# Kernel tuning notes

Hardware: AMD Instinct MI355X
Metric: run time of the kernel (lower is better)

Reference implementation:

```python
import jax, jax.numpy as jnp
import numpy as np

HORIZON_K = 20
EPS = 1e-8


def _unfold_gather(x, time_idx, k):
    # Emulates zero-pad + tensor.unfold(1, k, 1).permute(3,0,1,2) + index_select(2, time_idx)
    # x: [N, T-1, C] -> [k, N, S, C] where out[ki, n, s] = x_padded[n, time_idx[s] + ki]
    N, Tm1, C = x.shape
    xp = jnp.concatenate([x, jnp.zeros((N, k, C), x.dtype)], axis=1)
    gidx = time_idx[None, :] + jnp.arange(k)[:, None]  # [k, S]
    return jnp.transpose(xp[:, gidx, :], (1, 0, 2, 3))  # [k, N, S, C]


def _gru_rollout(x_seq, h0, W_ih, W_hh, b_ih, b_hh):
    # x_seq: [k, B, A]; h0: [B, H]; torch GRU gate order: r, z, n
    H = h0.shape[-1]
    def step(h, x):
        gi = x @ W_ih.T + b_ih          # [B, 3H]
        gh = h @ W_hh.T + b_hh          # [B, 3H]
        r = jax.nn.sigmoid(gi[:, :H] + gh[:, :H])
        z = jax.nn.sigmoid(gi[:, H:2 * H] + gh[:, H:2 * H])
        n = jnp.tanh(gi[:, 2 * H:] + r * gh[:, 2 * H:])
        hn = (1.0 - z) * n + z * h
        return hn, hn
    _, hs = jax.lax.scan(step, h0, x_seq)
    return hs  # [k, B, H]


def _mlp(x, W1, b1, W2, b2, W3, b3):
    x = jax.nn.relu(x @ W1 + b1)
    x = jax.nn.relu(x @ W2 + b2)
    return x @ W3 + b3


def _l2norm(x):
    n = jnp.linalg.norm(x, axis=-1, keepdims=True)
    return x / jnp.maximum(n, EPS)


def setup_inputs() -> dict:
    key = jax.random.key(0)
    ks = jax.random.split(key, 16)
    N, T, H, A, M = 1024, 128, 256, 18, 512
    g = lambda k, sh, s: jax.random.normal(k, sh, jnp.float32) * s
    return {
        "actions": jax.random.randint(ks[0], (N, T), 0, A),
        "dones": jnp.zeros((N, T), jnp.float32),
        "b_t": g(ks[1], (N * T, H), 1.0),
        "z_t": g(ks[2], (N * T, H), 1.0),
        "time_subsample": jax.random.randint(ks[3], (6,), 0, T - 1),
        "unroll_subsample": jax.random.randint(ks[4], (2,), 0, HORIZON_K),
        "W_ih": g(ks[5], (3 * H, A), 0.05), "W_hh": g(ks[6], (3 * H, H), 0.05),
        "b_ih": g(ks[7], (3 * H,), 0.05), "b_hh": g(ks[8], (3 * H,), 0.05),
        "W1": g(ks[9], (H, M), 0.05), "b1": g(ks[10], (M,), 0.05),
        "W2": g(ks[11], (M, M), 0.05), "b2": g(ks[12], (M,), 0.05),
        "W3": g(ks[13], (M, H), 0.05), "b3": g(ks[14], (H,), 0.05),
    }


def reference(actions, dones, b_t, z_t, time_subsample, unroll_subsample,
              W_ih, W_hh, b_ih, b_hh, W1, b1, W2, b2, W3, b3):
    N, T = actions.shape
    H = b_t.shape[-1]
    A = W_ih.shape[1]
    k = HORIZON_K

    # mask (dones fixed to all-zero -> max_k == horizon_k)
    not_dones = (1.0 - dones).reshape(N, T, 1)
    nd_unf = _unfold_gather(not_dones[:, :-1], time_subsample, k)        # [k,N,S,1]
    fmask = jnp.cumprod(nd_unf, axis=0).reshape(k, -1, 1)                # [k,N*S,1]
    fmask = (fmask[unroll_subsample] > 0).astype(jnp.float32)            # [F,B,1]

    # unfolded one-hot actions
    onehot = jax.nn.one_hot(actions, A, dtype=jnp.float32)               # [N,T,A]
    act_unf = _unfold_gather(onehot[:, :-1], time_subsample, k)          # [k,N,S,A]
    act_unf = act_unf.reshape(k, -1, A)                                  # [k,B,A]

    # GRU initial states from core outputs at subsampled times
    c = b_t.reshape(N, T, H)[:, :-1][:, time_subsample]                  # [N,S,H]
    h0 = c.reshape(-1, H)                                                # [B,H]

    # 20-step open-loop GRU rollout
    h_pred = _gru_rollout(act_unf, h0, W_ih, W_hh, b_ih, b_hh)           # [k,B,H]
    h_pred = h_pred[unroll_subsample]                                    # [F,B,H]

    final_pred = _mlp(h_pred, W1, b1, W2, b2, W3, b3)                    # [F,B,H]
    norm = jnp.linalg.norm(final_pred, axis=2)
    reg = 0.02 * jnp.square(norm - 1.0)                                  # [F,B]
    final_pred = _l2norm(final_pred)

    # targets (no grad): unfolded future encodings, normalized
    z = jax.lax.stop_gradient(z_t).reshape(N, T, -1)
    tgt = _unfold_gather(z[:, 1:], time_subsample, k)                    # [k,N,S,C]
    tgt = tgt[unroll_subsample].reshape(len(unroll_subsample), -1, z.shape[-1])
    tgt = _l2norm(tgt)                                                   # [F,B,C]

    loss = jnp.square(final_pred - tgt)                                  # [F,B,C]
    loss = loss.mean(-1, keepdims=True)                                  # [F,B,1]
    loss = jnp.sum(loss * fmask) / jnp.maximum(jnp.sum(fmask), 1.0)
    return loss + reg.mean()
```

## Files before the change

### kernel.cpp

```cpp
#include <hip/hip_runtime.h>
#include <hip/hip_bf16.h>
#include <math.h>

#define NN 1024
#define TT 128
#define SS 6
#define FF 2
#define HH 256
#define AA 18
#define MM 512
#define KH 20
#define BB (NN*SS)
#define RR (FF*BB)

#define SCL_RZ (-1.44269504089f)
#define SCL_N  (-2.88539008178f)
#define TBL_STRIDE 784

typedef __bf16 bf16x8 __attribute__((ext_vector_type(8)));
typedef float f32x4 __attribute__((ext_vector_type(4)));

__device__ __forceinline__ f32x4 mfma16(bf16x8 a, bf16x8 b, f32x4 c) {
    return __builtin_amdgcn_mfma_f32_16x16x32_bf16(a, b, c, 0, 0, 0);
}
__device__ __forceinline__ unsigned short f2b(float f) {
    return __builtin_bit_cast(unsigned short, __float2bfloat16(f));
}
__device__ __forceinline__ float b2f(unsigned short u) {
    return __builtin_bit_cast(float, (unsigned)u << 16);
}
__device__ __forceinline__ float rcp_f(float x)  { return __builtin_amdgcn_rcpf(x); }
__device__ __forceinline__ float exp2_f(float x) { return __builtin_amdgcn_exp2f(x); }

#define OFF_ACT   0UL
#define OFF_HPRED 491520UL
#define OFF_WHH   6782976UL
#define OFF_W1T   7176192UL
#define OFF_W2T   7438336UL
#define OFF_W3T   7962624UL
#define OFF_TBL   8224768UL
#define OFF_PART  8284352UL

__global__ void k_prep(const float* __restrict__ Whh, const float* __restrict__ W1,
                       const float* __restrict__ W2, const float* __restrict__ W3,
                       const float* __restrict__ Wih, const float* __restrict__ bih,
                       const float* __restrict__ bhh,
                       const int* __restrict__ actions, const int* __restrict__ ts,
                       unsigned short* whh_s, unsigned short* w1t, unsigned short* w2t,
                       unsigned short* w3t, float* tbl, int* act) {
    int idx = blockIdx.x * 256 + threadIdx.x;
    if (idx < 196608) {
        int wrow = idx >> 8;
        float scl = (wrow < 512) ? SCL_RZ : SCL_N;
        whh_s[idx] = f2b(Whh[idx] * scl);
        return;
    }
    idx -= 196608;
    if (idx < 131072) { int m = idx >> 8, k = idx & 255; w1t[idx] = f2b(W1[k * MM + m]); return; }
    idx -= 131072;
    if (idx < 262144) { int m = idx >> 9, k = idx & 511; w2t[idx] = f2b(W2[k * MM + m]); return; }
    idx -= 262144;
    if (idx < 131072) { int c = idx >> 9, k = idx & 511; w3t[idx] = f2b(W3[k * HH + c]); return; }
    idx -= 131072;
    if (idx < 19 * TBL_STRIDE) {
        int a = idx / TBL_STRIDE, rem = idx - a * TBL_STRIDE;
        float v = 0.f;
        if (rem < 768) {
            int g = rem >> 8;
            float scl = (g < 2) ? SCL_RZ : SCL_N;
            float w = (a < AA) ? Wih[rem * AA + a] : 0.f;
            v = scl * (w + bih[rem] + ((g < 2) ? bhh[rem] : 0.f));
        }
        tbl[idx] = v;
        return;
    }
    idx -= 19 * TBL_STRIDE;
    if (idx < BB * KH) {
        int b = idx / KH, k = idx - b * KH;
        int n = b / SS, s = b - n * SS;
        int tt = ts[s] + k;
        act[idx] = (tt < TT - 1) ? actions[n * TT + tt] : AA;
    }
}

__global__ void __launch_bounds__(512, 2)
k_gru_all(const unsigned short* __restrict__ whh_s, const float* __restrict__ tblg,
          const float* __restrict__ bhh, const int* __restrict__ actg,
          const int* __restrict__ us, const int* __restrict__ ts,
          const float* __restrict__ b_t, unsigned short* __restrict__ hpred) {
    __shared__ float tbl[19 * TBL_STRIDE];
    __shared__ unsigned short htile[2][32][264];
    __shared__ int act_l[24][KH];

    int tid = threadIdx.x, wave = tid >> 6, lane = tid & 63;
    int l15 = lane & 15, grp = lane >> 4, lk8 = grp << 3, r4 = grp << 2;
    int rb = blockIdx.x * 24;
    int u0 = us[0], u1 = us[1];
    int kmax = u0 > u1 ? u0 : u1;

    for (int i = tid; i < 19 * TBL_STRIDE / 4; i += 512)
        reinterpret_cast<float4*>(tbl)[i] = reinterpret_cast<const float4*>(tblg)[i];
    if (tid < 24 * KH) {
        int r = tid / KH, k2 = tid - r * KH;
        act_l[r][k2] = actg[(rb + r) * KH + k2];
    }

    for (int i = tid; i < 2 * 32 * 32; i += 512) {
        int buf = i >> 10, rem = i & 1023, row = rem >> 5, c8 = (rem & 31) << 3;
        uint4 pk = {0u, 0u, 0u, 0u};
        if (buf == 0 && row < 24) {
            int b = rb + row;
            int n = b / SS, s = b - n * SS;
            const float* src = &b_t[(size_t)(n * TT + ts[s]) * HH + c8];
            pk.x = f2b(src[0]) | ((unsigned)f2b(src[1]) << 16);
            pk.y = f2b(src[2]) | ((unsigned)f2b(src[3]) << 16);
            pk.z = f2b(src[4]) | ((unsigned)f2b(src[5]) << 16);
            pk.w = f2b(src[6]) | ((unsigned)f2b(src[7]) << 16);
        }
        *reinterpret_cast<uint4*>(&htile[buf][row][c8]) = pk;
    }

    bf16x8 wr[6][8];
#pragma unroll
    for (int ct = 0; ct < 6; ++ct) {
        int wrow = (ct >> 1) * 256 + wave * 32 + (ct & 1) * 16 + l15;
        const unsigned short* base = &whh_s[(size_t)wrow * HH];
#pragma unroll
        for (int kk = 0; kk < 8; ++kk)
            wr[ct][kk] = *reinterpret_cast<const bf16x8*>(&base[kk * 32 + lk8]);
    }
    float bhn[2];
#pragma unroll
    for (int cj = 0; cj < 2; ++cj) bhn[cj] = SCL_N * bhh[512 + wave * 32 + cj * 16 + l15];
    __syncthreads();

    int cur = 0;
    for (int ki = 0; ki <= kmax; ++ki) {
        int nxt = cur ^ 1;
#pragma unroll
        for (int rt = 0; rt < 2; ++rt) {
            f32x4 aR[2] = {}, aZ[2] = {}, aN[2] = {};
#pragma unroll
            for (int kk = 0; kk < 8; ++kk) {
                bf16x8 ah = *reinterpret_cast<const bf16x8*>(&htile[cur][rt * 16 + l15][kk * 32 + lk8]);
                aR[0] = mfma16(ah, wr[0][kk], aR[0]);
                aR[1] = mfma16(ah, wr[1][kk], aR[1]);
                aZ[0] = mfma16(ah, wr[2][kk], aZ[0]);
                aZ[1] = mfma16(ah, wr[3][kk], aZ[1]);
                aN[0] = mfma16(ah, wr[4][kk], aN[0]);
                aN[1] = mfma16(ah, wr[5][kk], aN[1]);
            }
#pragma unroll
            for (int cj = 0; cj < 2; ++cj) {
                int j2 = wave * 32 + cj * 16 + l15;
                float bhnv = bhn[cj];
#pragma unroll
                for (int reg = 0; reg < 4; ++reg) {
                    int rowl = rt * 16 + r4 + reg;
                    if (rt == 0 || rowl < 24) {
                        const float* tb = &tbl[act_l[rowl][ki] * TBL_STRIDE];
                        float r = rcp_f(1.f + exp2_f(aR[cj][reg] + tb[j2]));
                        float z = rcp_f(1.f + exp2_f(aZ[cj][reg] + tb[256 + j2]));
                        float ghn = aN[cj][reg] + bhnv;
                        float nv = 2.f * rcp_f(1.f + exp2_f(tb[512 + j2] + r * ghn)) - 1.f;
                        float h = b2f(htile[cur][rowl][j2]);
                        float hn2 = nv + z * (h - nv);
                        unsigned short hbv = f2b(hn2);
                        htile[nxt][rowl][j2] = hbv;
                        if (ki == u0) hpred[(size_t)(rb + rowl) * HH + j2] = hbv;
                        if (ki == u1) hpred[(size_t)(BB + rb + rowl) * HH + j2] = hbv;
                    }
                }
            }
        }
        __syncthreads();
        cur = nxt;
    }
}

__device__ __forceinline__ int xsw(int row, int chunk) {
    return (row << 9) + ((chunk ^ (row & 7)) << 3);
}

__global__ void __launch_bounds__(512, 4)
k_mlp_loss(const unsigned short* __restrict__ hpred, const unsigned short* __restrict__ w1t,
           const unsigned short* __restrict__ w2t, const unsigned short* __restrict__ w3t,
           const float* __restrict__ b1, const float* __restrict__ b2,
           const float* __restrict__ b3, const float* __restrict__ z_t,
           const float* __restrict__ dones, const int* __restrict__ ts,
           const int* __restrict__ us, float* __restrict__ part) {
    __shared__ unsigned short xs[48 * 512];
    __shared__ unsigned short zs[48 * 256];
    __shared__ float rstat[48][8][3];
    __shared__ float vmask[48];

    int tid = threadIdx.x, wave = tid >> 6, lane = tid & 63;
    int l15 = lane & 15, grp = lane >> 4, lk8 = grp << 3, r4 = grp << 2;
    int rb = blockIdx.x * 48;

    if (tid < 48) {
        int rg = rb + tid;
        int f = rg >= BB ? 1 : 0;
        int b = rg - f * BB;
        int n = b / SS, s = b - n * SS;
        int t = ts[s], u = us[f];
        float m = (t + u < TT - 1) ? 1.f : 0.f;
        if (m > 0.f) for (int j = 0; j <= u; ++j) m *= (1.f - dones[n * TT + t + j]);
        vmask[tid] = (m > 0.f) ? 1.f : 0.f;
    }
    for (int i = tid; i < 48 * 64; i += 512) {
        int row = i >> 6, c4 = (i & 63) << 2;
        int rg = rb + row;
        int f = rg >= BB ? 1 : 0;
        int b = rg - f * BB;
        int n = b / SS, s = b - n * SS;
        int t = ts[s], u = us[f];
        uint2 pk = {0u, 0u};
        if (t + u < TT - 1) {
            float4 v = *reinterpret_cast<const float4*>(&z_t[(size_t)(n * TT + 1 + t + u) * HH + c4]);
            pk.x = f2b(v.x) | ((unsigned)f2b(v.y) << 16);
            pk.y = f2b(v.z) | ((unsigned)f2b(v.w) << 16);
        }
        *reinterpret_cast<uint2*>(&zs[row * 256 + c4]) = pk;
    }

    {
        f32x4 acc[3][4] = {};
        for (int kk = 0; kk < 8; ++kk) {
            int k0 = kk * 32 + lk8;
            bf16x8 av[3];
#pragma unroll
            for (int rt = 0; rt < 3; ++rt)
                av[rt] = *reinterpret_cast<const bf16x8*>(&hpred[(size_t)(rb + rt * 16 + l15) * HH + k0]);
#pragma unroll
            for (int ct = 0; ct < 4; ++ct) {
                int col = wave * 64 + ct * 16 + l15;
                bf16x8 bv = *reinterpret_cast<const bf16x8*>(&w1t[(size_t)col * HH + k0]);
#pragma unroll
                for (int rt = 0; rt < 3; ++rt) acc[rt][ct] = mfma16(av[rt], bv, acc[rt][ct]);
            }
        }
#pragma unroll
        for (int ct = 0; ct < 4; ++ct) {
            int col = wave * 64 + ct * 16 + l15;
            float bb = b1[col];
#pragma unroll
            for (int rt = 0; rt < 3; ++rt)
#pragma unroll
                for (int reg = 0; reg < 4; ++reg)
                    xs[xsw(rt * 16 + r4 + reg, col >> 3) + (col & 7)] =
                        f2b(fmaxf(acc[rt][ct][reg] + bb, 0.f));
        }
    }
    __syncthreads();

    {
        f32x4 acc[3][4] = {};
        for (int kk = 0; kk < 16; ++kk) {
            bf16x8 av[3];
#pragma unroll
            for (int rt = 0; rt < 3; ++rt)
                av[rt] = *reinterpret_cast<const bf16x8*>(&xs[xsw(rt * 16 + l15, kk * 4 + grp)]);
#pragma unroll
            for (int ct = 0; ct < 4; ++ct) {
                int col = wave * 64 + ct * 16 + l15;
                bf16x8 bv = *reinterpret_cast<const bf16x8*>(&w2t[(size_t)col * MM + kk * 32 + lk8]);
#pragma unroll
                for (int rt = 0; rt < 3; ++rt) acc[rt][ct] = mfma16(av[rt], bv, acc[rt][ct]);
            }
        }
        __syncthreads();
#pragma unroll
        for (int ct = 0; ct < 4; ++ct) {
            int col = wave * 64 + ct * 16 + l15;
            float bb = b2[col];
#pragma unroll
            for (int rt = 0; rt < 3; ++rt)
#pragma unroll
                for (int reg = 0; reg < 4; ++reg)
                    xs[xsw(rt * 16 + r4 + reg, col >> 3) + (col & 7)] =
                        f2b(fmaxf(acc[rt][ct][reg] + bb, 0.f));
        }
    }
    __syncthreads();

    {
        f32x4 acc[3][2] = {};
        for (int kk = 0; kk < 16; ++kk) {
            bf16x8 av[3];
#pragma unroll
            for (int rt = 0; rt < 3; ++rt)
                av[rt] = *reinterpret_cast<const bf16x8*>(&xs[xsw(rt * 16 + l15, kk * 4 + grp)]);
#pragma unroll
            for (int ct = 0; ct < 2; ++ct) {
                int col = wave * 32 + ct * 16 + l15;
                bf16x8 bv = *reinterpret_cast<const bf16x8*>(&w3t[(size_t)col * MM + kk * 32 + lk8]);
#pragma unroll
                for (int rt = 0; rt < 3; ++rt) acc[rt][ct] = mfma16(av[rt], bv, acc[rt][ct]);
            }
        }
        float b3c0 = b3[wave * 32 + l15];
        float b3c1 = b3[wave * 32 + 16 + l15];
#pragma unroll
        for (int rt = 0; rt < 3; ++rt)
#pragma unroll
            for (int reg = 0; reg < 4; ++reg) {
                int row = rt * 16 + r4 + reg;
                float p0 = acc[rt][0][reg] + b3c0;
                float p1 = acc[rt][1][reg] + b3c1;
                float z0 = b2f(zs[row * 256 + wave * 32 + l15]);
                float z1 = b2f(zs[row * 256 + wave * 32 + 16 + l15]);
                float psq = p0 * p0 + p1 * p1;
                float zsq = z0 * z0 + z1 * z1;
                float pz  = p0 * z0 + p1 * z1;
#pragma unroll
                for (int o = 1; o < 16; o <<= 1) {
                    psq += __shfl_xor(psq, o);
                    zsq += __shfl_xor(zsq, o);
                    pz  += __shfl_xor(pz, o);
                }
                if (l15 == 0) {
                    rstat[row][wave][0] = psq;
                    rstat[row][wave][1] = zsq;
                    rstat[row][wave][2] = pz;
                }
            }
    }
    __syncthreads();

    if (tid < 64) {
        float a0 = 0.f, a1 = 0.f, a2 = 0.f;
        if (tid < 48) {
            float sp = 0.f, sz = 0.f, spz = 0.f;
#pragma unroll
            for (int w = 0; w < 8; ++w) {
                sp  += rstat[tid][w][0];
                sz  += rstat[tid][w][1];
                spz += rstat[tid][w][2];
            }
            float npn = sqrtf(sp), nzn = sqrtf(sz);
            float d = npn - 1.f;
            a2 = 0.02f * d * d;
            float mp = fmaxf(npn, 1e-8f), mz = fmaxf(nzn, 1e-8f);
            float lossr = (sp / (mp * mp) + sz / (mz * mz) - 2.f * spz / (mp * mz)) * (1.f / HH);
            float vm = vmask[tid];
            a0 = vm * lossr;
            a1 = vm;
        }
#pragma unroll
        for (int o = 1; o < 64; o <<= 1) {
            a0 += __shfl_xor(a0, o);
            a1 += __shfl_xor(a1, o);
            a2 += __shfl_xor(a2, o);
        }
        if (tid == 0) {
            part[blockIdx.x * 3 + 0] = a0;
            part[blockIdx.x * 3 + 1] = a1;
            part[blockIdx.x * 3 + 2] = a2;
        }
    }
}

__global__ void k_final(const float* __restrict__ part, float* out) {
    int tid = threadIdx.x, wave = tid >> 6, lane = tid & 63;
    float s0 = 0.f, s1 = 0.f, s2 = 0.f;
    for (int i = tid; i < 256; i += 256) {
        s0 += part[i * 3 + 0];
        s1 += part[i * 3 + 1];
        s2 += part[i * 3 + 2];
    }
    for (int o = 32; o; o >>= 1) {
        s0 += __shfl_xor(s0, o);
        s1 += __shfl_xor(s1, o);
        s2 += __shfl_xor(s2, o);
    }
    __shared__ float sm[4][3];
    if (lane == 0) { sm[wave][0] = s0; sm[wave][1] = s1; sm[wave][2] = s2; }
    __syncthreads();
    if (tid == 0) {
        float a = 0.f, b = 0.f, c = 0.f;
        for (int w = 0; w < 4; ++w) { a += sm[w][0]; b += sm[w][1]; c += sm[w][2]; }
        out[0] = a / fmaxf(b, 1.f) + c * (1.f / RR);
    }
}

extern "C" void kernel_launch(void* const* d_in, const int* in_sizes, int n_in,
                              void* d_out, int out_size, void* d_ws, size_t ws_size,
                              hipStream_t stream) {
    const int*   actions = (const int*)d_in[0];
    const float* dones   = (const float*)d_in[1];
    const float* b_t     = (const float*)d_in[2];
    const float* z_t     = (const float*)d_in[3];
    const int*   ts      = (const int*)d_in[4];
    const int*   us      = (const int*)d_in[5];
    const float* W_ih    = (const float*)d_in[6];
    const float* W_hh    = (const float*)d_in[7];
    const float* b_ih    = (const float*)d_in[8];
    const float* b_hh    = (const float*)d_in[9];
    const float* W1      = (const float*)d_in[10];
    const float* b1      = (const float*)d_in[11];
    const float* W2      = (const float*)d_in[12];
    const float* b2      = (const float*)d_in[13];
    const float* W3      = (const float*)d_in[14];
    const float* b3      = (const float*)d_in[15];

    char* ws = (char*)d_ws;
    int*            act   = (int*)(ws + OFF_ACT);
    unsigned short* hpred = (unsigned short*)(ws + OFF_HPRED);
    unsigned short* whh_s = (unsigned short*)(ws + OFF_WHH);
    unsigned short* w1t   = (unsigned short*)(ws + OFF_W1T);
    unsigned short* w2t   = (unsigned short*)(ws + OFF_W2T);
    unsigned short* w3t   = (unsigned short*)(ws + OFF_W3T);
    float*          tbl   = (float*)(ws + OFF_TBL);
    float*          part  = (float*)(ws + OFF_PART);

    k_prep<<<3355, 256, 0, stream>>>(W_hh, W1, W2, W3, W_ih, b_ih, b_hh, actions, ts,
                                     whh_s, w1t, w2t, w3t, tbl, act);
    k_gru_all<<<256, 512, 0, stream>>>(whh_s, tbl, b_hh, act, us, ts, b_t, hpred);
    k_mlp_loss<<<256, 512, 0, stream>>>(hpred, w1t, w2t, w3t, b1, b2, b3,
                                        z_t, dones, ts, us, part);
    k_final<<<1, 256, 0, stream>>>(part, (float*)d_out);
}
```

Before: 115.1 us.

## Compute GRU input gates via one-hot MFMA instead of LDS lookup table

Replaces the ~60KB shared-memory W_ih/bias lookup table with a bf16 packed W_ih (bias folded in as an extra column). The input-gate contributions are now produced by MFMA against a one-hot action vector built in registers. It also reassigns output columns so each lane owns two adjacent hidden units, keeps the fp32 hidden state in registers instead of re-reading bf16 from LDS, and writes packed 32-bit stores. The goal is to free LDS for occupancy and remove gather loads from the recurrence, at the cost of extra MFMAs per step and bf16 rounding of the input weights.

```diff
diff --git a/kernel.cpp b/kernel.cpp
--- a/kernel.cpp
+++ b/kernel.cpp
@@ -15,10 +15,10 @@
 
 #define SCL_RZ (-1.44269504089f)
 #define SCL_N  (-2.88539008178f)
-#define TBL_STRIDE 784
 
 typedef __bf16 bf16x8 __attribute__((ext_vector_type(8)));
 typedef float f32x4 __attribute__((ext_vector_type(4)));
+typedef unsigned ux4 __attribute__((ext_vector_type(4)));
 
 __device__ __forceinline__ f32x4 mfma16(bf16x8 a, bf16x8 b, f32x4 c) {
     return __builtin_amdgcn_mfma_f32_16x16x32_bf16(a, b, c, 0, 0, 0);
@@ -38,8 +38,8 @@
 #define OFF_W1T   7176192UL
 #define OFF_W2T   7438336UL
 #define OFF_W3T   7962624UL
-#define OFF_TBL   8224768UL
-#define OFF_PART  8284352UL
+#define OFF_WIHP  8224768UL
+#define OFF_PART  8273920UL
 
 __global__ void k_prep(const float* __restrict__ Whh, const float* __restrict__ W1,
                        const float* __restrict__ W2, const float* __restrict__ W3,
@@ -47,7 +47,7 @@
                        const float* __restrict__ bhh,
                        const int* __restrict__ actions, const int* __restrict__ ts,
                        unsigned short* whh_s, unsigned short* w1t, unsigned short* w2t,
-                       unsigned short* w3t, float* tbl, int* act) {
+                       unsigned short* w3t, unsigned short* wihp, int* act_t) {
     int idx = blockIdx.x * 256 + threadIdx.x;
     if (idx < 196608) {
         int wrow = idx >> 8;
@@ -62,48 +62,68 @@
     idx -= 262144;
     if (idx < 131072) { int c = idx >> 9, k = idx & 511; w3t[idx] = f2b(W3[k * HH + c]); return; }
     idx -= 131072;
-    if (idx < 19 * TBL_STRIDE) {
-        int a = idx / TBL_STRIDE, rem = idx - a * TBL_STRIDE;
+    if (idx < 24576) {
+        int c = idx >> 5, k = idx & 31;
+        int g = c >> 8;
+        float scl = (g < 2) ? SCL_RZ : SCL_N;
         float v = 0.f;
-        if (rem < 768) {
-            int g = rem >> 8;
-            float scl = (g < 2) ? SCL_RZ : SCL_N;
-            float w = (a < AA) ? Wih[rem * AA + a] : 0.f;
-            v = scl * (w + bih[rem] + ((g < 2) ? bhh[rem] : 0.f));
-        }
-        tbl[idx] = v;
+        if (k < AA) v = scl * Wih[c * AA + k];
+        else if (k == AA) v = scl * (bih[c] + ((g < 2) ? bhh[c] : 0.f));
+        wihp[idx] = f2b(v);
         return;
     }
-    idx -= 19 * TBL_STRIDE;
-    if (idx < BB * KH) {
-        int b = idx / KH, k = idx - b * KH;
+    idx -= 24576;
+    if (idx < KH * BB) {
+        int ki = idx / BB, b = idx - ki * BB;
         int n = b / SS, s = b - n * SS;
-        int tt = ts[s] + k;
-        act[idx] = (tt < TT - 1) ? actions[n * TT + tt] : AA;
+        int tt = ts[s] + ki;
+        act_t[idx] = (tt < TT - 1) ? actions[n * TT + tt] : AA;
     }
 }
 
 __global__ void __launch_bounds__(512, 2)
-k_gru_all(const unsigned short* __restrict__ whh_s, const float* __restrict__ tblg,
-          const float* __restrict__ bhh, const int* __restrict__ actg,
+k_gru_all(const unsigned short* __restrict__ whh_s, const unsigned short* __restrict__ wihp,
+          const float* __restrict__ bhh, const int* __restrict__ act_t,
           const int* __restrict__ us, const int* __restrict__ ts,
           const float* __restrict__ b_t, unsigned short* __restrict__ hpred) {
-    __shared__ float tbl[19 * TBL_STRIDE];
-    __shared__ unsigned short htile[2][32][264];
-    __shared__ int act_l[24][KH];
+    __shared__ alignas(16) unsigned short htile[2][32][264];
 
     int tid = threadIdx.x, wave = tid >> 6, lane = tid & 63;
     int l15 = lane & 15, grp = lane >> 4, lk8 = grp << 3, r4 = grp << 2;
     int rb = blockIdx.x * 24;
     int u0 = us[0], u1 = us[1];
     int kmax = u0 > u1 ? u0 : u1;
-
-    for (int i = tid; i < 19 * TBL_STRIDE / 4; i += 512)
-        reinterpret_cast<float4*>(tbl)[i] = reinterpret_cast<const float4*>(tblg)[i];
-    if (tid < 24 * KH) {
-        int r = tid / KH, k2 = tid - r * KH;
-        act_l[r][k2] = actg[(rb + r) * KH + k2];
-    }
+    int j0 = wave * 32 + 2 * l15;
+
+    bf16x8 wr[6][8];
+    bf16x8 wih[6];
+#pragma unroll
+    for (int ct = 0; ct < 6; ++ct) {
+        int wrow = (ct >> 1) * 256 + j0 + (ct & 1);
+        const unsigned short* base = &whh_s[(size_t)wrow * HH];
+#pragma unroll
+        for (int kk = 0; kk < 8; ++kk)
+            wr[ct][kk] = *reinterpret_cast<const bf16x8*>(&base[kk * 32 + lk8]);
+        wih[ct] = *reinterpret_cast<const bf16x8*>(&wihp[wrow * 32 + lk8]);
+    }
+    float bhn0 = SCL_N * bhh[512 + j0];
+    float bhn1 = SCL_N * bhh[512 + j0 + 1];
+
+    float hm[2][2][4];
+#pragma unroll
+    for (int rt = 0; rt < 2; ++rt)
+#pragma unroll
+        for (int reg = 0; reg < 4; ++reg) {
+            int rowl = rt * 16 + r4 + reg;
+            float v0 = 0.f, v1 = 0.f;
+            if (rowl < 24) {
+                int b = rb + rowl;
+                int n = b / SS, s = b - n * SS;
+                const float* src = &b_t[(size_t)(n * TT + ts[s]) * HH + j0];
+                v0 = src[0]; v1 = src[1];
+            }
+            hm[rt][0][reg] = v0; hm[rt][1][reg] = v1;
+        }
 
     for (int i = tid; i < 2 * 32 * 32; i += 512) {
         int buf = i >> 10, rem = i & 1023, row = rem >> 5, c8 = (rem & 31) << 3;
@@ -119,57 +139,60 @@
         }
         *reinterpret_cast<uint4*>(&htile[buf][row][c8]) = pk;
     }
-
-    bf16x8 wr[6][8];
-#pragma unroll
-    for (int ct = 0; ct < 6; ++ct) {
-        int wrow = (ct >> 1) * 256 + wave * 32 + (ct & 1) * 16 + l15;
-        const unsigned short* base = &whh_s[(size_t)wrow * HH];
-#pragma unroll
-        for (int kk = 0; kk < 8; ++kk)
-            wr[ct][kk] = *reinterpret_cast<const bf16x8*>(&base[kk * 32 + lk8]);
-    }
-    float bhn[2];
-#pragma unroll
-    for (int cj = 0; cj < 2; ++cj) bhn[cj] = SCL_N * bhh[512 + wave * 32 + cj * 16 + l15];
     __syncthreads();
 
     int cur = 0;
     for (int ki = 0; ki <= kmax; ++ki) {
         int nxt = cur ^ 1;
+        int a0 = act_t[ki * BB + rb + l15];
+        int i1 = rb + 16 + l15;
+        int a1 = act_t[ki * BB + (i1 < BB ? i1 : BB - 1)];
+
 #pragma unroll
         for (int rt = 0; rt < 2; ++rt) {
-            f32x4 aR[2] = {}, aZ[2] = {}, aN[2] = {};
+            int a = rt ? a1 : a0;
+            ux4 ohu;
+#pragma unroll
+            for (int i = 0; i < 4; ++i) {
+                int k0 = lk8 + 2 * i, k1 = k0 + 1;
+                unsigned v0 = (a == k0 || k0 == AA) ? 0x3F80u : 0u;
+                unsigned v1 = (a == k1 || k1 == AA) ? 0x3F80u : 0u;
+                ohu[i] = v0 | (v1 << 16);
+            }
+            bf16x8 ohf = __builtin_bit_cast(bf16x8, ohu);
+
+            f32x4 aR0 = {}, aR1 = {}, aZ0 = {}, aZ1 = {}, aN0 = {}, aN1 = {}, aNI0 = {}, aNI1 = {};
+            aR0  = mfma16(ohf, wih[0], aR0);  aR1  = mfma16(ohf, wih[1], aR1);
+            aZ0  = mfma16(ohf, wih[2], aZ0);  aZ1  = mfma16(ohf, wih[3], aZ1);
+            aNI0 = mfma16(ohf, wih[4], aNI0); aNI1 = mfma16(ohf, wih[5], aNI1);
 #pragma unroll
             for (int kk = 0; kk < 8; ++kk) {
                 bf16x8 ah = *reinterpret_cast<const bf16x8*>(&htile[cur][rt * 16 + l15][kk * 32 + lk8]);
-                aR[0] = mfma16(ah, wr[0][kk], aR[0]);
-                aR[1] = mfma16(ah, wr[1][kk], aR[1]);
-                aZ[0] = mfma16(ah, wr[2][kk], aZ[0]);
-                aZ[1] = mfma16(ah, wr[3][kk], aZ[1]);
-                aN[0] = mfma16(ah, wr[4][kk], aN[0]);
-                aN[1] = mfma16(ah, wr[5][kk], aN[1]);
-            }
-#pragma unroll
-            for (int cj = 0; cj < 2; ++cj) {
-                int j2 = wave * 32 + cj * 16 + l15;
-                float bhnv = bhn[cj];
-#pragma unroll
-                for (int reg = 0; reg < 4; ++reg) {
-                    int rowl = rt * 16 + r4 + reg;
-                    if (rt == 0 || rowl < 24) {
-                        const float* tb = &tbl[act_l[rowl][ki] * TBL_STRIDE];
-                        float r = rcp_f(1.f + exp2_f(aR[cj][reg] + tb[j2]));
-                        float z = rcp_f(1.f + exp2_f(aZ[cj][reg] + tb[256 + j2]));
-                        float ghn = aN[cj][reg] + bhnv;
-                        float nv = 2.f * rcp_f(1.f + exp2_f(tb[512 + j2] + r * ghn)) - 1.f;
-                        float h = b2f(htile[cur][rowl][j2]);
-                        float hn2 = nv + z * (h - nv);
-                        unsigned short hbv = f2b(hn2);
-                        htile[nxt][rowl][j2] = hbv;
-                        if (ki == u0) hpred[(size_t)(rb + rowl) * HH + j2] = hbv;
-                        if (ki == u1) hpred[(size_t)(BB + rb + rowl) * HH + j2] = hbv;
-                    }
+                aR0 = mfma16(ah, wr[0][kk], aR0); aR1 = mfma16(ah, wr[1][kk], aR1);
+                aZ0 = mfma16(ah, wr[2][kk], aZ0); aZ1 = mfma16(ah, wr[3][kk], aZ1);
+                aN0 = mfma16(ah, wr[4][kk], aN0); aN1 = mfma16(ah, wr[5][kk], aN1);
+            }
+#pragma unroll
+            for (int reg = 0; reg < 4; ++reg) {
+                int rowl = rt * 16 + r4 + reg;
+                float r0 = rcp_f(1.f + exp2_f(aR0[reg]));
+                float r1 = rcp_f(1.f + exp2_f(aR1[reg]));
+                float z0 = rcp_f(1.f + exp2_f(aZ0[reg]));
+                float z1 = rcp_f(1.f + exp2_f(aZ1[reg]));
+                float tv0 = aNI0[reg] + r0 * (aN0[reg] + bhn0);
+                float tv1 = aNI1[reg] + r1 * (aN1[reg] + bhn1);
+                float nv0 = 2.f * rcp_f(1.f + exp2_f(tv0)) - 1.f;
+                float nv1 = 2.f * rcp_f(1.f + exp2_f(tv1)) - 1.f;
+                float h0n = nv0 + z0 * (hm[rt][0][reg] - nv0);
+                float h1n = nv1 + z1 * (hm[rt][1][reg] - nv1);
+                hm[rt][0][reg] = h0n; hm[rt][1][reg] = h1n;
+                if (rowl < 24) {
+                    unsigned hv = (unsigned)f2b(h0n) | ((unsigned)f2b(h1n) << 16);
+                    *reinterpret_cast<unsigned*>(&htile[nxt][rowl][j0]) = hv;
+                    if (ki == u0)
+                        *reinterpret_cast<unsigned*>(&hpred[(size_t)(rb + rowl) * HH + j0]) = hv;
+                    if (ki == u1)
+                        *reinterpret_cast<unsigned*>(&hpred[(size_t)(BB + rb + rowl) * HH + j0]) = hv;
                 }
             }
         }
@@ -364,10 +387,10 @@
 __global__ void k_final(const float* __restrict__ part, float* out) {
     int tid = threadIdx.x, wave = tid >> 6, lane = tid & 63;
     float s0 = 0.f, s1 = 0.f, s2 = 0.f;
-    for (int i = tid; i < 256; i += 256) {
-        s0 += part[i * 3 + 0];
-        s1 += part[i * 3 + 1];
-        s2 += part[i * 3 + 2];
+    if (tid < 256) {
+        s0 = part[tid * 3 + 0];
+        s1 = part[tid * 3 + 1];
+        s2 = part[tid * 3 + 2];
     }
     for (int o = 32; o; o >>= 1) {
         s0 += __shfl_xor(s0, o);
@@ -405,18 +428,18 @@
     const float* b3      = (const float*)d_in[15];
 
     char* ws = (char*)d_ws;
-    int*            act   = (int*)(ws + OFF_ACT);
+    int*            act_t = (int*)(ws + OFF_ACT);
     unsigned short* hpred = (unsigned short*)(ws + OFF_HPRED);
     unsigned short* whh_s = (unsigned short*)(ws + OFF_WHH);
     unsigned short* w1t   = (unsigned short*)(ws + OFF_W1T);
     unsigned short* w2t   = (unsigned short*)(ws + OFF_W2T);
     unsigned short* w3t   = (unsigned short*)(ws + OFF_W3T);
-    float*          tbl   = (float*)(ws + OFF_TBL);
+    unsigned short* wihp  = (unsigned short*)(ws + OFF_WIHP);
     float*          part  = (float*)(ws + OFF_PART);
 
-    k_prep<<<3355, 256, 0, stream>>>(W_hh, W1, W2, W3, W_ih, b_ih, b_hh, actions, ts,
-                                     whh_s, w1t, w2t, w3t, tbl, act);
-    k_gru_all<<<256, 512, 0, stream>>>(whh_s, tbl, b_hh, act, us, ts, b_t, hpred);
+    k_prep<<<3392, 256, 0, stream>>>(W_hh, W1, W2, W3, W_ih, b_ih, b_hh, actions, ts,
+                                     whh_s, w1t, w2t, w3t, wihp, act_t);
+    k_gru_all<<<256, 512, 0, stream>>>(whh_s, wihp, b_hh, act_t, us, ts, b_t, hpred);
     k_mlp_loss<<<256, 512, 0, stream>>>(hpred, w1t, w2t, w3t, b1, b2, b3,
                                         z_t, dones, ts, us, part);
     k_final<<<1, 256, 0, stream>>>(part, (float*)d_out);
```

After: 133.9 us. 1.16x slower.

## Shrink GRU blocks to 16 rows, keep hidden state in fp32 registers

Applied to the files above, without the earlier changes.

The GRU rollout kernel now handles 16 batch rows per block instead of 24, which removes the wasted half-filled second MFMA row tile and raises the grid from 256 to 384 blocks to spread work across more CUs. The hidden state is carried in fp32 registers rather than reread from a bf16 LDS tile, and the double-buffered tile is replaced by one buffer with an extra barrier between the MFMA reads and the writes. This trades an added sync per step and a repeated per-block table load for better CU utilisation, and may slightly change numerics because h no longer round-trips through bf16. k_final is also simplified to a direct load per thread.

```diff
diff --git a/kernel.cpp b/kernel.cpp
--- a/kernel.cpp
+++ b/kernel.cpp
@@ -89,35 +89,20 @@
           const int* __restrict__ us, const int* __restrict__ ts,
           const float* __restrict__ b_t, unsigned short* __restrict__ hpred) {
     __shared__ float tbl[19 * TBL_STRIDE];
-    __shared__ unsigned short htile[2][32][264];
-    __shared__ int act_l[24][KH];
+    __shared__ int act_l[16][KH];
+    __shared__ unsigned short htile[16][264];
 
     int tid = threadIdx.x, wave = tid >> 6, lane = tid & 63;
     int l15 = lane & 15, grp = lane >> 4, lk8 = grp << 3, r4 = grp << 2;
-    int rb = blockIdx.x * 24;
+    int rb = blockIdx.x * 16;
     int u0 = us[0], u1 = us[1];
     int kmax = u0 > u1 ? u0 : u1;
 
     for (int i = tid; i < 19 * TBL_STRIDE / 4; i += 512)
         reinterpret_cast<float4*>(tbl)[i] = reinterpret_cast<const float4*>(tblg)[i];
-    if (tid < 24 * KH) {
-        int r = tid / KH, k2 = tid - r * KH;
-        act_l[r][k2] = actg[(rb + r) * KH + k2];
-    }
-
-    for (int i = tid; i < 2 * 32 * 32; i += 512) {
-        int buf = i >> 10, rem = i & 1023, row = rem >> 5, c8 = (rem & 31) << 3;
-        uint4 pk = {0u, 0u, 0u, 0u};
-        if (buf == 0 && row < 24) {
-            int b = rb + row;
-            int n = b / SS, s = b - n * SS;
-            const float* src = &b_t[(size_t)(n * TT + ts[s]) * HH + c8];
-            pk.x = f2b(src[0]) | ((unsigned)f2b(src[1]) << 16);
-            pk.y = f2b(src[2]) | ((unsigned)f2b(src[3]) << 16);
-            pk.z = f2b(src[4]) | ((unsigned)f2b(src[5]) << 16);
-            pk.w = f2b(src[6]) | ((unsigned)f2b(src[7]) << 16);
-        }
-        *reinterpret_cast<uint4*>(&htile[buf][row][c8]) = pk;
+    if (tid < 16 * KH) {
+        int r = tid / KH, k = tid - r * KH;
+        act_l[r][k] = actg[(rb + r) * KH + k];
     }
 
     bf16x8 wr[6][8];
@@ -129,52 +114,70 @@
         for (int kk = 0; kk < 8; ++kk)
             wr[ct][kk] = *reinterpret_cast<const bf16x8*>(&base[kk * 32 + lk8]);
     }
+
+    float hm[2][4];
+#pragma unroll
+    for (int cj = 0; cj < 2; ++cj)
+#pragma unroll
+        for (int reg = 0; reg < 4; ++reg) {
+            int b = rb + r4 + reg;
+            int n = b / SS, s = b - n * SS;
+            hm[cj][reg] = b_t[(size_t)(n * TT + ts[s]) * HH + wave * 32 + cj * 16 + l15];
+        }
     float bhn[2];
 #pragma unroll
     for (int cj = 0; cj < 2; ++cj) bhn[cj] = SCL_N * bhh[512 + wave * 32 + cj * 16 + l15];
+
+    {
+        int row = tid >> 5, c8 = (tid & 31) << 3;
+        int b = rb + row;
+        int n = b / SS, s = b - n * SS;
+        const float* src = &b_t[(size_t)(n * TT + ts[s]) * HH + c8];
+        uint4 pk;
+        pk.x = f2b(src[0]) | ((unsigned)f2b(src[1]) << 16);
+        pk.y = f2b(src[2]) | ((unsigned)f2b(src[3]) << 16);
+        pk.z = f2b(src[4]) | ((unsigned)f2b(src[5]) << 16);
+        pk.w = f2b(src[6]) | ((unsigned)f2b(src[7]) << 16);
+        *reinterpret_cast<uint4*>(&htile[row][c8]) = pk;
+    }
     __syncthreads();
 
-    int cur = 0;
     for (int ki = 0; ki <= kmax; ++ki) {
-        int nxt = cur ^ 1;
-#pragma unroll
-        for (int rt = 0; rt < 2; ++rt) {
-            f32x4 aR[2] = {}, aZ[2] = {}, aN[2] = {};
-#pragma unroll
-            for (int kk = 0; kk < 8; ++kk) {
-                bf16x8 ah = *reinterpret_cast<const bf16x8*>(&htile[cur][rt * 16 + l15][kk * 32 + lk8]);
-                aR[0] = mfma16(ah, wr[0][kk], aR[0]);
-                aR[1] = mfma16(ah, wr[1][kk], aR[1]);
-                aZ[0] = mfma16(ah, wr[2][kk], aZ[0]);
-                aZ[1] = mfma16(ah, wr[3][kk], aZ[1]);
-                aN[0] = mfma16(ah, wr[4][kk], aN[0]);
-                aN[1] = mfma16(ah, wr[5][kk], aN[1]);
-            }
-#pragma unroll
-            for (int cj = 0; cj < 2; ++cj) {
-                int j2 = wave * 32 + cj * 16 + l15;
-                float bhnv = bhn[cj];
-#pragma unroll
-                for (int reg = 0; reg < 4; ++reg) {
-                    int rowl = rt * 16 + r4 + reg;
-                    if (rt == 0 || rowl < 24) {
-                        const float* tb = &tbl[act_l[rowl][ki] * TBL_STRIDE];
-                        float r = rcp_f(1.f + exp2_f(aR[cj][reg] + tb[j2]));
-                        float z = rcp_f(1.f + exp2_f(aZ[cj][reg] + tb[256 + j2]));
-                        float ghn = aN[cj][reg] + bhnv;
-                        float nv = 2.f * rcp_f(1.f + exp2_f(tb[512 + j2] + r * ghn)) - 1.f;
-                        float h = b2f(htile[cur][rowl][j2]);
-                        float hn2 = nv + z * (h - nv);
-                        unsigned short hbv = f2b(hn2);
-                        htile[nxt][rowl][j2] = hbv;
-                        if (ki == u0) hpred[(size_t)(rb + rowl) * HH + j2] = hbv;
-                        if (ki == u1) hpred[(size_t)(BB + rb + rowl) * HH + j2] = hbv;
-                    }
-                }
-            }
+        f32x4 aR[2] = {}, aZ[2] = {}, aN[2] = {};
+#pragma unroll
+        for (int kk = 0; kk < 8; ++kk) {
+            bf16x8 ah = *reinterpret_cast<const bf16x8*>(&htile[l15][kk * 32 + lk8]);
+            aR[0] = mfma16(ah, wr[0][kk], aR[0]);
+            aR[1] = mfma16(ah, wr[1][kk], aR[1]);
+            aZ[0] = mfma16(ah, wr[2][kk], aZ[0]);
+            aZ[1] = mfma16(ah, wr[3][kk], aZ[1]);
+            aN[0] = mfma16(ah, wr[4][kk], aN[0]);
+            aN[1] = mfma16(ah, wr[5][kk], aN[1]);
         }
         __syncthreads();
-        cur = nxt;
+
+#pragma unroll
+        for (int cj = 0; cj < 2; ++cj) {
+            int j2 = wave * 32 + cj * 16 + l15;
+            float bhnv = bhn[cj];
+#pragma unroll
+            for (int reg = 0; reg < 4; ++reg) {
+                int row = r4 + reg;
+                const float* tb = &tbl[act_l[row][ki] * TBL_STRIDE];
+                float r = rcp_f(1.f + exp2_f(aR[cj][reg] + tb[j2]));
+                float z = rcp_f(1.f + exp2_f(aZ[cj][reg] + tb[256 + j2]));
+                float ghn = aN[cj][reg] + bhnv;
+                float nv = 2.f * rcp_f(1.f + exp2_f(tb[512 + j2] + r * ghn)) - 1.f;
+                float h = hm[cj][reg];
+                float hn2 = nv + z * (h - nv);
+                hm[cj][reg] = hn2;
+                unsigned short hbv = f2b(hn2);
+                htile[row][j2] = hbv;
+                if (ki == u0) hpred[(size_t)(rb + row) * HH + j2] = hbv;
+                if (ki == u1) hpred[(size_t)(BB + rb + row) * HH + j2] = hbv;
+            }
+        }
+        __syncthreads();
     }
 }
 
@@ -205,7 +208,7 @@
         int n = b / SS, s = b - n * SS;
         int t = ts[s], u = us[f];
         float m = (t + u < TT - 1) ? 1.f : 0.f;
-        if (m > 0.f) for (int j = 0; j <= u; ++j) m *= (1.f - dones[n * TT + t + j]);
+        if (m > 0.f) for (int jj = 0; jj <= u; ++jj) m *= (1.f - dones[n * TT + t + jj]);
         vmask[tid] = (m > 0.f) ? 1.f : 0.f;
     }
     for (int i = tid; i < 48 * 64; i += 512) {
@@ -363,12 +366,9 @@
 
 __global__ void k_final(const float* __restrict__ part, float* out) {
     int tid = threadIdx.x, wave = tid >> 6, lane = tid & 63;
-    float s0 = 0.f, s1 = 0.f, s2 = 0.f;
-    for (int i = tid; i < 256; i += 256) {
-        s0 += part[i * 3 + 0];
-        s1 += part[i * 3 + 1];
-        s2 += part[i * 3 + 2];
-    }
+    float s0 = part[tid * 3 + 0];
+    float s1 = part[tid * 3 + 1];
+    float s2 = part[tid * 3 + 2];
     for (int o = 32; o; o >>= 1) {
         s0 += __shfl_xor(s0, o);
         s1 += __shfl_xor(s1, o);
@@ -416,7 +416,7 @@
 
     k_prep<<<3355, 256, 0, stream>>>(W_hh, W1, W2, W3, W_ih, b_ih, b_hh, actions, ts,
                                      whh_s, w1t, w2t, w3t, tbl, act);
-    k_gru_all<<<256, 512, 0, stream>>>(whh_s, tbl, b_hh, act, us, ts, b_t, hpred);
+    k_gru_all<<<384, 512, 0, stream>>>(whh_s, tbl, b_hh, act, us, ts, b_t, hpred);
     k_mlp_loss<<<256, 512, 0, stream>>>(hpred, w1t, w2t, w3t, b1, b2, b3,
                                         z_t, dones, ts, us, part);
     k_final<<<1, 256, 0, stream>>>(part, (float*)d_out);
```

New measurement: 125.2 us. +8.8%, slower.

## Pack GRU input-gate table as bf16 pairs and keep hidden state in registers

Applied to the files above, without the earlier changes.

Remaps the GRU weight rows so each lane owns two adjacent hidden columns, and stores the per-action input-gate table as packed bf16 pairs in one uint4 per column pair. The per-step gate epilogue then needs one LDS vector load instead of three scalar float loads, and writes 32-bit packed hidden values. The previous hidden value is kept in registers rather than reread from LDS. This shrinks the LDS table and the per-step LDS traffic, at the cost of rounding the gate bias table to bf16 and adding some register pressure.

```diff
diff --git a/kernel.cpp b/kernel.cpp
--- a/kernel.cpp
+++ b/kernel.cpp
@@ -15,7 +15,7 @@
 
 #define SCL_RZ (-1.44269504089f)
 #define SCL_N  (-2.88539008178f)
-#define TBL_STRIDE 784
+#define TBLP_STRIDE 129
 
 typedef __bf16 bf16x8 __attribute__((ext_vector_type(8)));
 typedef float f32x4 __attribute__((ext_vector_type(4)));
@@ -28,6 +28,12 @@
 }
 __device__ __forceinline__ float b2f(unsigned short u) {
     return __builtin_bit_cast(float, (unsigned)u << 16);
+}
+__device__ __forceinline__ float blo(unsigned u) {
+    return __builtin_bit_cast(float, u << 16);
+}
+__device__ __forceinline__ float bhi(unsigned u) {
+    return __builtin_bit_cast(float, u & 0xffff0000u);
 }
 __device__ __forceinline__ float rcp_f(float x)  { return __builtin_amdgcn_rcpf(x); }
 __device__ __forceinline__ float exp2_f(float x) { return __builtin_amdgcn_exp2f(x); }
@@ -39,7 +45,7 @@
 #define OFF_W2T   7438336UL
 #define OFF_W3T   7962624UL
 #define OFF_TBL   8224768UL
-#define OFF_PART  8284352UL
+#define OFF_PART  8264000UL
 
 __global__ void k_prep(const float* __restrict__ Whh, const float* __restrict__ W1,
                        const float* __restrict__ W2, const float* __restrict__ W3,
@@ -47,7 +53,7 @@
                        const float* __restrict__ bhh,
                        const int* __restrict__ actions, const int* __restrict__ ts,
                        unsigned short* whh_s, unsigned short* w1t, unsigned short* w2t,
-                       unsigned short* w3t, float* tbl, int* act) {
+                       unsigned short* w3t, uint4* tblp, int* act) {
     int idx = blockIdx.x * 256 + threadIdx.x;
     if (idx < 196608) {
         int wrow = idx >> 8;
@@ -62,19 +68,31 @@
     idx -= 262144;
     if (idx < 131072) { int c = idx >> 9, k = idx & 511; w3t[idx] = f2b(W3[k * HH + c]); return; }
     idx -= 131072;
-    if (idx < 19 * TBL_STRIDE) {
-        int a = idx / TBL_STRIDE, rem = idx - a * TBL_STRIDE;
-        float v = 0.f;
-        if (rem < 768) {
-            int g = rem >> 8;
-            float scl = (g < 2) ? SCL_RZ : SCL_N;
-            float w = (a < AA) ? Wih[rem * AA + a] : 0.f;
-            v = scl * (w + bih[rem] + ((g < 2) ? bhh[rem] : 0.f));
-        }
-        tbl[idx] = v;
+    if (idx < 19 * TBLP_STRIDE) {
+        int a = idx / TBLP_STRIDE, jp = idx - a * TBLP_STRIDE;
+        uint4 o = {0u, 0u, 0u, 0u};
+        if (jp < 128) {
+            int j0 = jp * 2, j1 = j0 + 1;
+            float wr0 = (a < AA) ? Wih[j0 * AA + a] : 0.f;
+            float wr1 = (a < AA) ? Wih[j1 * AA + a] : 0.f;
+            float wz0 = (a < AA) ? Wih[(256 + j0) * AA + a] : 0.f;
+            float wz1 = (a < AA) ? Wih[(256 + j1) * AA + a] : 0.f;
+            float wn0 = (a < AA) ? Wih[(512 + j0) * AA + a] : 0.f;
+            float wn1 = (a < AA) ? Wih[(512 + j1) * AA + a] : 0.f;
+            float r0 = SCL_RZ * (wr0 + bih[j0] + bhh[j0]);
+            float r1 = SCL_RZ * (wr1 + bih[j1] + bhh[j1]);
+            float z0 = SCL_RZ * (wz0 + bih[256 + j0] + bhh[256 + j0]);
+            float z1 = SCL_RZ * (wz1 + bih[256 + j1] + bhh[256 + j1]);
+            float n0 = SCL_N * (wn0 + bih[512 + j0]);
+            float n1 = SCL_N * (wn1 + bih[512 + j1]);
+            o.x = (unsigned)f2b(r0) | ((unsigned)f2b(r1) << 16);
+            o.y = (unsigned)f2b(z0) | ((unsigned)f2b(z1) << 16);
+            o.z = (unsigned)f2b(n0) | ((unsigned)f2b(n1) << 16);
+        }
+        tblp[idx] = o;
         return;
     }
-    idx -= 19 * TBL_STRIDE;
+    idx -= 19 * TBLP_STRIDE;
     if (idx < BB * KH) {
         int b = idx / KH, k = idx - b * KH;
         int n = b / SS, s = b - n * SS;
@@ -84,26 +102,55 @@
 }
 
 __global__ void __launch_bounds__(512, 2)
-k_gru_all(const unsigned short* __restrict__ whh_s, const float* __restrict__ tblg,
+k_gru_all(const unsigned short* __restrict__ whh_s, const uint4* __restrict__ tblpg,
           const float* __restrict__ bhh, const int* __restrict__ actg,
           const int* __restrict__ us, const int* __restrict__ ts,
           const float* __restrict__ b_t, unsigned short* __restrict__ hpred) {
-    __shared__ float tbl[19 * TBL_STRIDE];
-    __shared__ unsigned short htile[2][32][264];
-    __shared__ int act_l[24][KH];
+    __shared__ uint4 tbl[19 * TBLP_STRIDE];
+    __shared__ alignas(16) unsigned short htile[2][32][264];
+    __shared__ int act_l[32][KH];
 
     int tid = threadIdx.x, wave = tid >> 6, lane = tid & 63;
     int l15 = lane & 15, grp = lane >> 4, lk8 = grp << 3, r4 = grp << 2;
     int rb = blockIdx.x * 24;
     int u0 = us[0], u1 = us[1];
     int kmax = u0 > u1 ? u0 : u1;
-
-    for (int i = tid; i < 19 * TBL_STRIDE / 4; i += 512)
-        reinterpret_cast<float4*>(tbl)[i] = reinterpret_cast<const float4*>(tblg)[i];
-    if (tid < 24 * KH) {
+    int j0 = wave * 32 + 2 * l15;
+    int jp = wave * 16 + l15;
+
+    for (int i = tid; i < 19 * TBLP_STRIDE; i += 512) tbl[i] = tblpg[i];
+    if (tid < 32 * KH) {
         int r = tid / KH, k2 = tid - r * KH;
-        act_l[r][k2] = actg[(rb + r) * KH + k2];
-    }
+        act_l[r][k2] = (r < 24) ? actg[(rb + r) * KH + k2] : AA;
+    }
+
+    bf16x8 wr[6][8];
+#pragma unroll
+    for (int ct = 0; ct < 6; ++ct) {
+        int wrow = (ct >> 1) * 256 + j0 + (ct & 1);
+        const unsigned short* base = &whh_s[(size_t)wrow * HH];
+#pragma unroll
+        for (int kk = 0; kk < 8; ++kk)
+            wr[ct][kk] = *reinterpret_cast<const bf16x8*>(&base[kk * 32 + lk8]);
+    }
+    float bhn0 = SCL_N * bhh[512 + j0];
+    float bhn1 = SCL_N * bhh[512 + j0 + 1];
+
+    unsigned hmp[2][4];
+#pragma unroll
+    for (int rt = 0; rt < 2; ++rt)
+#pragma unroll
+        for (int reg = 0; reg < 4; ++reg) {
+            int rowl = rt * 16 + r4 + reg;
+            unsigned hv = 0u;
+            if (rowl < 24) {
+                int b = rb + rowl;
+                int n = b / SS, s = b - n * SS;
+                const float* src = &b_t[(size_t)(n * TT + ts[s]) * HH + j0];
+                hv = (unsigned)f2b(src[0]) | ((unsigned)f2b(src[1]) << 16);
+            }
+            hmp[rt][reg] = hv;
+        }
 
     for (int i = tid; i < 2 * 32 * 32; i += 512) {
         int buf = i >> 10, rem = i & 1023, row = rem >> 5, c8 = (rem & 31) << 3;
@@ -119,19 +166,6 @@
         }
         *reinterpret_cast<uint4*>(&htile[buf][row][c8]) = pk;
     }
-
-    bf16x8 wr[6][8];
-#pragma unroll
-    for (int ct = 0; ct < 6; ++ct) {
-        int wrow = (ct >> 1) * 256 + wave * 32 + (ct & 1) * 16 + l15;
-        const unsigned short* base = &whh_s[(size_t)wrow * HH];
-#pragma unroll
-        for (int kk = 0; kk < 8; ++kk)
-            wr[ct][kk] = *reinterpret_cast<const bf16x8*>(&base[kk * 32 + lk8]);
-    }
-    float bhn[2];
-#pragma unroll
-    for (int cj = 0; cj < 2; ++cj) bhn[cj] = SCL_N * bhh[512 + wave * 32 + cj * 16 + l15];
     __syncthreads();
 
     int cur = 0;
@@ -151,25 +185,28 @@
                 aN[1] = mfma16(ah, wr[5][kk], aN[1]);
             }
 #pragma unroll
-            for (int cj = 0; cj < 2; ++cj) {
-                int j2 = wave * 32 + cj * 16 + l15;
-                float bhnv = bhn[cj];
-#pragma unroll
-                for (int reg = 0; reg < 4; ++reg) {
-                    int rowl = rt * 16 + r4 + reg;
-                    if (rt == 0 || rowl < 24) {
-                        const float* tb = &tbl[act_l[rowl][ki] * TBL_STRIDE];
-                        float r = rcp_f(1.f + exp2_f(aR[cj][reg] + tb[j2]));
-                        float z = rcp_f(1.f + exp2_f(aZ[cj][reg] + tb[256 + j2]));
-                        float ghn = aN[cj][reg] + bhnv;
-                        float nv = 2.f * rcp_f(1.f + exp2_f(tb[512 + j2] + r * ghn)) - 1.f;
-                        float h = b2f(htile[cur][rowl][j2]);
-                        float hn2 = nv + z * (h - nv);
-                        unsigned short hbv = f2b(hn2);
-                        htile[nxt][rowl][j2] = hbv;
-                        if (ki == u0) hpred[(size_t)(rb + rowl) * HH + j2] = hbv;
-                        if (ki == u1) hpred[(size_t)(BB + rb + rowl) * HH + j2] = hbv;
-                    }
+            for (int reg = 0; reg < 4; ++reg) {
+                int rowl = rt * 16 + r4 + reg;
+                uint4 gi = tbl[act_l[rowl][ki] * TBLP_STRIDE + jp];
+                float r0 = rcp_f(1.f + exp2_f(aR[0][reg] + blo(gi.x)));
+                float r1 = rcp_f(1.f + exp2_f(aR[1][reg] + bhi(gi.x)));
+                float z0 = rcp_f(1.f + exp2_f(aZ[0][reg] + blo(gi.y)));
+                float z1 = rcp_f(1.f + exp2_f(aZ[1][reg] + bhi(gi.y)));
+                float tv0 = blo(gi.z) + r0 * (aN[0][reg] + bhn0);
+                float tv1 = bhi(gi.z) + r1 * (aN[1][reg] + bhn1);
+                float nv0 = 2.f * rcp_f(1.f + exp2_f(tv0)) - 1.f;
+                float nv1 = 2.f * rcp_f(1.f + exp2_f(tv1)) - 1.f;
+                unsigned hp = hmp[rt][reg];
+                float hn0 = nv0 + z0 * (blo(hp) - nv0);
+                float hn1 = nv1 + z1 * (bhi(hp) - nv1);
+                unsigned hv = (unsigned)f2b(hn0) | ((unsigned)f2b(hn1) << 16);
+                hmp[rt][reg] = hv;
+                if (rowl < 24) {
+                    *reinterpret_cast<unsigned*>(&htile[nxt][rowl][j0]) = hv;
+                    if (ki == u0)
+                        *reinterpret_cast<unsigned*>(&hpred[(size_t)(rb + rowl) * HH + j0]) = hv;
+                    if (ki == u1)
+                        *reinterpret_cast<unsigned*>(&hpred[(size_t)(BB + rb + rowl) * HH + j0]) = hv;
                 }
             }
         }
@@ -205,7 +242,7 @@
         int n = b / SS, s = b - n * SS;
         int t = ts[s], u = us[f];
         float m = (t + u < TT - 1) ? 1.f : 0.f;
-        if (m > 0.f) for (int j = 0; j <= u; ++j) m *= (1.f - dones[n * TT + t + j]);
+        if (m > 0.f) for (int jj = 0; jj <= u; ++jj) m *= (1.f - dones[n * TT + t + jj]);
         vmask[tid] = (m > 0.f) ? 1.f : 0.f;
     }
     for (int i = tid; i < 48 * 64; i += 512) {
@@ -363,12 +400,9 @@
 
 __global__ void k_final(const float* __restrict__ part, float* out) {
     int tid = threadIdx.x, wave = tid >> 6, lane = tid & 63;
-    float s0 = 0.f, s1 = 0.f, s2 = 0.f;
-    for (int i = tid; i < 256; i += 256) {
-        s0 += part[i * 3 + 0];
-        s1 += part[i * 3 + 1];
-        s2 += part[i * 3 + 2];
-    }
+    float s0 = part[tid * 3 + 0];
+    float s1 = part[tid * 3 + 1];
+    float s2 = part[tid * 3 + 2];
     for (int o = 32; o; o >>= 1) {
         s0 += __shfl_xor(s0, o);
         s1 += __shfl_xor(s1, o);
@@ -411,12 +445,12 @@
     unsigned short* w1t   = (unsigned short*)(ws + OFF_W1T);
     unsigned short* w2t   = (unsigned short*)(ws + OFF_W2T);
     unsigned short* w3t   = (unsigned short*)(ws + OFF_W3T);
-    float*          tbl   = (float*)(ws + OFF_TBL);
+    uint4*          tblp  = (uint4*)(ws + OFF_TBL);
     float*          part  = (float*)(ws + OFF_PART);
 
-    k_prep<<<3355, 256, 0, stream>>>(W_hh, W1, W2, W3, W_ih, b_ih, b_hh, actions, ts,
-                                     whh_s, w1t, w2t, w3t, tbl, act);
-    k_gru_all<<<256, 512, 0, stream>>>(whh_s, tbl, b_hh, act, us, ts, b_t, hpred);
+    k_prep<<<3306, 256, 0, stream>>>(W_hh, W1, W2, W3, W_ih, b_ih, b_hh, actions, ts,
+                                     whh_s, w1t, w2t, w3t, tblp, act);
+    k_gru_all<<<256, 512, 0, stream>>>(whh_s, tblp, b_hh, act, us, ts, b_t, hpred);
     k_mlp_loss<<<256, 512, 0, stream>>>(hpred, w1t, w2t, w3t, b1, b2, b3,
                                         z_t, dones, ts, us, part);
     k_final<<<1, 256, 0, stream>>>(part, (float*)d_out);
```

Result: no change. 116.4 us (+1.2%).
